# Performance work log

Hardware: AMD Instinct MI355X
Metric: run time of the kernel (lower is better)

## Reference

```python
import jax, jax.numpy as jnp
import numpy as np

DIM = 1024
HEAD_DIM = 64
CHUNK = 128
B, T = 4, 4096


def setup_inputs() -> dict:
    key = jax.random.key(0)
    ks = jax.random.split(key, 8)
    s = 1.0 / np.sqrt(DIM)
    inp = {
        'x': jax.random.normal(ks[0], (B, T, DIM), jnp.float32),
        'Wq': jax.random.normal(ks[1], (DIM, DIM), jnp.float32) * s,
        'bq': jnp.zeros((DIM,), jnp.float32),
        'Wk': jax.random.normal(ks[2], (DIM, DIM), jnp.float32) * s,
        'bk': jnp.zeros((DIM,), jnp.float32),
        'Wv': jax.random.normal(ks[3], (DIM, DIM), jnp.float32) * s,
        'bv': jnp.zeros((DIM,), jnp.float32),
        'Wbeta': jax.random.normal(ks[4], (DIM, DIM), jnp.float32) * s,
        'bbeta': jnp.zeros((DIM,), jnp.float32),
        'Walpha': jax.random.normal(ks[5], (DIM, DIM), jnp.float32) * s,
        'balpha': jnp.full((DIM,), 2.0, jnp.float32),  # bias init 2.0 as in torch
    }
    return inp


def reference(x, Wq, bq, Wk, bk, Wv, bv, Wbeta, bbeta, Walpha, balpha):
    Bsz, Tlen, D = x.shape
    d = HEAD_DIM
    H = D // d
    C = CHUNK
    scale = d ** (-0.5)

    q = ((x @ Wq.T + bq) * scale).reshape(Bsz, Tlen, H, d)
    k = ((x @ Wk.T + bk) * scale).reshape(Bsz, Tlen, H, d)
    v = (x @ Wv.T + bv).reshape(Bsz, Tlen, H, d)
    alpha_logits = jnp.clip((x @ Walpha.T + balpha).reshape(Bsz, Tlen, H, d), -10.0, 10.0)
    log_alpha = jax.nn.log_sigmoid(alpha_logits)
    alpha_val = jax.nn.sigmoid(alpha_logits)
    beta = jax.nn.softplus(x @ Wbeta.T + bbeta).reshape(Bsz, Tlen, H, d)

    # pad T to a multiple of C (static)
    pad = (-Tlen) % C
    if pad:
        pw = ((0, 0), (0, pad), (0, 0), (0, 0))
        q, k, v = jnp.pad(q, pw), jnp.pad(k, pw), jnp.pad(v, pw)
        log_alpha, beta = jnp.pad(log_alpha, pw), jnp.pad(beta, pw)
    N = q.shape[1] // C
    cshape = (Bsz, N, C, H, d)
    q, k, v = q.reshape(cshape), k.reshape(cshape), v.reshape(cshape)
    log_alpha, beta = log_alpha.reshape(cshape), beta.reshape(cshape)

    ccum = jnp.cumsum(log_alpha, axis=2)          # (B,N,C,H,d)
    m = ccum.mean(axis=-1)                        # (B,N,C,H); mean is linear -> take before pairwise diff
    decay_logits_mean = m[:, :, :, None, :] - m[:, :, None, :, :]  # (B,N,C,C,H)
    tril = jnp.tril(jnp.ones((C, C), jnp.float32))[None, None, :, :, None]
    decay_logits_mean = jnp.where(tril == 0, -1e9, decay_logits_mean)
    decay = jnp.exp(decay_logits_mean)            # (B,N,C,C,H)

    attn = jnp.einsum('bnihd,bnjhd->bnhij', q, k)
    attn = attn * decay.transpose(0, 1, 4, 2, 3)
    y_intra = jnp.einsum('bnhij,bnjhd->bnihd', attn, v * beta)  # (B,N,C,H,d)

    # inter-chunk recurrence via scan over chunks
    asum = jnp.exp(log_alpha.sum(axis=2).mean(axis=-1))  # (B,N,H) total chunk decay
    curve = jnp.exp(m)                                   # (B,N,C,H) intra-chunk decay curve
    bmean = beta.mean(axis=-1)                           # (B,N,C,H)

    def to_scan(a):
        return jnp.moveaxis(a, 1, 0)
    xs = (to_scan(q), to_scan(y_intra), to_scan(curve), to_scan(asum),
          to_scan(k), to_scan(v), to_scan(bmean))

    state0 = jnp.zeros((Bsz, H, d, d), jnp.float32)

    def step(state, inputs):
        qi, yi, ci, ai, ki, vi, bmi = inputs
        mem = jnp.einsum('bchq,bhqk->bchk', qi, state)
        y = yi + mem * ci[..., None]
        state = state * ai[:, :, None, None]
        delta = jnp.einsum('bchk,bchv,bch->bhkv', ki, vi, bmi)
        return state + delta, y

    state, ys = jax.lax.scan(step, state0, xs)
    y = jnp.moveaxis(ys, 0, 1).reshape(Bsz, N * C, D)
    if pad:
        y = y[:, :Tlen, :]
    return y, state, alpha_val
```

## Files before the change

kernel.cpp:

```cpp
#include <hip/hip_runtime.h>
#include <cstdint>
#include <cmath>

#define DIMM 1024
#define NHEAD 16
#define HEADD 64
#define CHUNKC 128
#define NBATCH 4
#define TLEN 4096
#define NCHUNK 32
#define BT (NBATCH * TLEN)
#define NSTACK (5 * DIMM)

typedef unsigned short ushort_t;
typedef __attribute__((ext_vector_type(8))) short short8;
typedef __attribute__((ext_vector_type(4))) float f32x4;

__device__ __forceinline__ float blo(unsigned int u) { return __uint_as_float(u << 16); }
__device__ __forceinline__ float bhi(unsigned int u) { return __uint_as_float(u & 0xffff0000u); }
__device__ __forceinline__ ushort_t f2bf(float f) {
  unsigned int u = __float_as_uint(f);
  u += 0x7fffu + ((u >> 16) & 1u);
  return (ushort_t)(u >> 16);
}
__device__ __forceinline__ float bf2f(ushort_t s) { return __uint_as_float(((unsigned int)s) << 16); }
__device__ __forceinline__ unsigned pack2(float a, float b) {
  return (unsigned)f2bf(a) | ((unsigned)f2bf(b) << 16);
}

__device__ __forceinline__ void stage16(unsigned lds_base, const ushort_t* g) {
  asm volatile("s_mov_b32 m0, %0\n\t"
               "global_load_lds_dwordx4 %1, off"
               :: "s"(lds_base), "v"((unsigned long long)(size_t)g)
               : "memory");
}

__global__ __launch_bounds__(256) void k_cast(
    const float* __restrict__ x,
    const float* __restrict__ Wq, const float* __restrict__ Wk,
    const float* __restrict__ Wv, const float* __restrict__ Wb, const float* __restrict__ Wa,
    const float* __restrict__ bq, const float* __restrict__ bk,
    const float* __restrict__ bv, const float* __restrict__ bb, const float* __restrict__ ba,
    ushort_t* __restrict__ xb, ushort_t* __restrict__ wbm, float* __restrict__ bias_st) {
  const long XU = (long)BT * DIMM / 4;
  const long WU = (long)NSTACK * DIMM / 4;
  const long BU = NSTACK / 4;
  const long NU = XU + WU + BU;
  for (long u = (long)blockIdx.x * blockDim.x + threadIdx.x; u < NU;
       u += (long)gridDim.x * blockDim.x) {
    if (u < XU) {
      float4 f = ((const float4*)x)[u];
      ushort4 o;
      o.x = f2bf(f.x); o.y = f2bf(f.y); o.z = f2bf(f.z); o.w = f2bf(f.w);
      ((ushort4*)xb)[u] = o;
    } else if (u < XU + WU) {
      long j = u - XU;
      long e = j * 4;
      int row = (int)(e >> 10);
      int col = (int)(e & 1023);
      int p = row >> 10, wr = row & 1023;
      const float* Wp = (p == 0) ? Wq : (p == 1) ? Wk : (p == 2) ? Wv : (p == 3) ? Wb : Wa;
      float4 f = *(const float4*)(Wp + (size_t)wr * DIMM + col);
      ushort4 o;
      o.x = f2bf(f.x); o.y = f2bf(f.y); o.z = f2bf(f.z); o.w = f2bf(f.w);
      ((ushort4*)wbm)[j] = o;
    } else {
      long j = u - XU - WU;
      int e = (int)(j * 4);
      int p = e >> 10, r = e & 1023;
      const float* bp = (p == 0) ? bq : (p == 1) ? bk : (p == 2) ? bv : (p == 3) ? bb : ba;
      ((float4*)bias_st)[j] = *(const float4*)(bp + r);
    }
  }
}

#define BARR __builtin_amdgcn_s_barrier()
#define VMC0 asm volatile("s_waitcnt vmcnt(0)" ::: "memory")

#define STAGEP(bb, kt) do {                                                      \
    const size_t _ko = (size_t)(kt) * 32;                                        \
    unsigned _base = (unsigned)__builtin_amdgcn_readfirstlane(                   \
        (int)(unsigned)(size_t)((__attribute__((address_space(3))) char*)smem    \
                                + (bb) * 16384 + wv1024));                       \
    stage16(_base,         agb + _ko);                                           \
    stage16(_base + 4096,  agb + (size_t)64 * DIMM + _ko);                       \
    stage16(_base + 8192,  bgb + _ko);                                           \
    stage16(_base + 12288, bgb + (size_t)64 * DIMM + _ko);                       \
  } while (0)

__global__ __launch_bounds__(256) void k_proj(
    const ushort_t* __restrict__ xb, const ushort_t* __restrict__ wbm,
    const float* __restrict__ bias_st,
    ushort_t* __restrict__ qo, ushort_t* __restrict__ ko,
    ushort_t* __restrict__ vo, ushort_t* __restrict__ bo,
    float* __restrict__ ao) {
  __shared__ __align__(16) char smem[32768];
  const int tid = threadIdx.x;
  const int lane = tid & 63;
  const int wave = tid >> 6;
  const int quad = lane >> 4, lr = lane & 15;
  const int wr = (wave >> 1) * 64, wc = (wave & 1) * 64;
  const int sx = (lr >> 1) & 3;
  const int wv1024 = wave * 1024;

  const int bm0 = blockIdx.y * 128, bn0 = blockIdx.x * 128;

  const int trow = tid >> 2;
  const int gcol = (((tid & 3) ^ ((tid >> 3) & 3)) << 3);
  const ushort_t* agb = xb + (size_t)(bm0 + trow) * DIMM + gcol;
  const ushort_t* bgb = wbm + (size_t)(bn0 + trow) * DIMM + gcol;

  f32x4 zero = {0.f, 0.f, 0.f, 0.f};
  f32x4 acc[4][4];
#pragma unroll
  for (int i = 0; i < 4; ++i)
#pragma unroll
    for (int j = 0; j < 4; ++j) acc[i][j] = zero;

  STAGEP(0, 0);

#pragma unroll 2
  for (int kk = 0; kk < 32; ++kk) {
    VMC0;
    BARR;
    if (kk < 31) STAGEP((kk + 1) & 1, kk + 1);
    const char* Ab = smem + (kk & 1) * 16384;
    const char* Bb = Ab + 8192;
    short8 af[4], bfr[4];
#pragma unroll
    for (int i = 0; i < 4; ++i)
      af[i] = *(const short8*)(Ab + (wr + i * 16 + lr) * 64 + ((quad ^ sx) << 4));
#pragma unroll
    for (int j = 0; j < 4; ++j)
      bfr[j] = *(const short8*)(Bb + (wc + j * 16 + lr) * 64 + ((quad ^ sx) << 4));
#pragma unroll
    for (int i = 0; i < 4; ++i)
#pragma unroll
      for (int j = 0; j < 4; ++j)
        acc[i][j] = __builtin_amdgcn_mfma_f32_16x16x32_bf16(af[i], bfr[j], acc[i][j], 0, 0, 0);
  }

  const int p_id = bn0 >> 10;
  const int ncol0 = bn0 & 1023;

  if (p_id == 4) {
#pragma unroll
    for (int j = 0; j < 4; ++j) {
      const int colg = wc + j * 16 + lr;
      const float bias = bias_st[bn0 + colg];
      const int nc = ncol0 + colg;
#pragma unroll
      for (int i = 0; i < 4; ++i)
#pragma unroll
        for (int r = 0; r < 4; ++r) {
          const int rowl = wr + i * 16 + quad * 4 + r;
          float val = acc[i][j][r] + bias;
          float c = fminf(fmaxf(val, -10.f), 10.f);
          ao[(size_t)(bm0 + rowl) * DIMM + nc] = 1.f / (1.f + expf(-c));
        }
    }
  } else {
    ushort_t* outp = (p_id == 0) ? qo : (p_id == 1) ? ko : (p_id == 2) ? vo : bo;
    const float scl = (p_id <= 1) ? 0.125f : 1.f;
    ushort_t* T = (ushort_t*)smem;
    const int halfb = (wr == 64) ? 32 : 0;
#pragma unroll
    for (int pass = 0; pass < 2; ++pass) {
      __syncthreads();
#pragma unroll
      for (int ii = 0; ii < 2; ++ii) {
        const int i = pass * 2 + ii;
#pragma unroll
        for (int j = 0; j < 4; ++j) {
          const int col = wc + j * 16 + lr;
          const float bias = bias_st[bn0 + col];
#pragma unroll
          for (int r = 0; r < 4; ++r) {
            float val = acc[i][j][r] + bias;
            float ov;
            if (p_id == 3) ov = (val > 20.f) ? val : log1pf(expf(val));
            else ov = val * scl;
            T[(halfb + ii * 16 + quad * 4 + r) * 136 + col] = f2bf(ov);
          }
        }
      }
      __syncthreads();
      const int trw = tid >> 2;
      const int cch = (tid & 3) * 32;
      const int growl = pass * 32 + (trw & 31) + (trw >> 5) * 64;
      ushort_t* dst = outp + (size_t)(bm0 + growl) * DIMM + ncol0 + cch;
      const ushort_t* src = T + trw * 136 + cch;
#pragma unroll
      for (int u = 0; u < 4; ++u)
        *(uint4*)(dst + u * 8) = *(const uint4*)(src + u * 8);
    }
  }
}

#undef STAGEP
#undef BARR
#undef VMC0

__global__ __launch_bounds__(128) void k_stats(
    const float* __restrict__ alpha, const ushort_t* __restrict__ betaw,
    float* __restrict__ mArr, float* __restrict__ bmean, float* __restrict__ asum) {
  const int bnh = blockIdx.x;
  const int h = bnh & 15, n = (bnh >> 4) & 31, b = bnh >> 9;
  const int c = threadIdx.x;
  const size_t bt = (size_t)b * TLEN + n * CHUNKC + c;

  const float4* ap = (const float4*)(alpha + bt * DIMM + h * HEADD);
  float ls = 0.f;
#pragma unroll
  for (int w = 0; w < 16; ++w) {
    float4 a = ap[w];
    ls += logf(a.x) + logf(a.y) + logf(a.z) + logf(a.w);
  }
  const uint4* bp = (const uint4*)(betaw + bt * DIMM + h * HEADD);
  float bs = 0.f;
#pragma unroll
  for (int w = 0; w < 8; ++w) {
    uint4 u = bp[w];
    bs += blo(u.x) + bhi(u.x) + blo(u.y) + bhi(u.y) + blo(u.z) + bhi(u.z) + blo(u.w) + bhi(u.w);
  }
  float la = ls * (1.f / 64.f);

  __shared__ float s[128];
  s[c] = la;
  __syncthreads();
  for (int off = 1; off < 128; off <<= 1) {
    float t = (c >= off) ? s[c - off] : 0.f;
    __syncthreads();
    s[c] += t;
    __syncthreads();
  }
  float m = s[c];
  const size_t o = (size_t)bnh * CHUNKC + c;
  mArr[o] = m;
  bmean[o] = bs * (1.f / 64.f);
  if (c == 127) asum[bnh] = expf(m);
}

__global__ __launch_bounds__(256) void k_delta(
    const ushort_t* __restrict__ kw, const ushort_t* __restrict__ vw,
    const float* __restrict__ bmean, float* __restrict__ delta) {
  __shared__ ushort_t kc[8192];
  __shared__ ushort_t vc[8192];
  __shared__ float bm[128];
  const int bnh = blockIdx.x;
  const int h = bnh & 15, n = (bnh >> 4) & 31, b = bnh >> 9;
  const int tid = threadIdx.x;
  const size_t bt0 = (size_t)b * TLEN + n * CHUNKC;

#pragma unroll
  for (int it = 0; it < 4; ++it) {
    int u = tid + it * 256;
    int row = u >> 3, col = (u & 7) * 8;
    size_t go = (bt0 + row) * DIMM + h * HEADD + col;
    ((uint4*)kc)[u] = *(const uint4*)(kw + go);
    ((uint4*)vc)[u] = *(const uint4*)(vw + go);
  }
  if (tid < 128) bm[tid] = bmean[(size_t)bnh * CHUNKC + tid];
  __syncthreads();

  const int kd = tid >> 2, v0 = (tid & 3) * 16;
  float acc[16];
#pragma unroll
  for (int l = 0; l < 16; ++l) acc[l] = 0.f;

#pragma unroll 4
  for (int c = 0; c < 128; ++c) {
    float kb = bf2f(kc[c * 64 + kd]) * bm[c];
    const uint4* vr = (const uint4*)(vc + c * 64 + v0);
    uint4 u0 = vr[0], u1 = vr[1];
    acc[0] += kb * blo(u0.x);  acc[1] += kb * bhi(u0.x);
    acc[2] += kb * blo(u0.y);  acc[3] += kb * bhi(u0.y);
    acc[4] += kb * blo(u0.z);  acc[5] += kb * bhi(u0.z);
    acc[6] += kb * blo(u0.w);  acc[7] += kb * bhi(u0.w);
    acc[8] += kb * blo(u1.x);  acc[9] += kb * bhi(u1.x);
    acc[10] += kb * blo(u1.y); acc[11] += kb * bhi(u1.y);
    acc[12] += kb * blo(u1.z); acc[13] += kb * bhi(u1.z);
    acc[14] += kb * blo(u1.w); acc[15] += kb * bhi(u1.w);
  }
  float* dst = delta + (size_t)bnh * 4096 + kd * 64 + v0;
#pragma unroll
  for (int l4 = 0; l4 < 4; ++l4)
    ((float4*)dst)[l4] = make_float4(acc[l4 * 4], acc[l4 * 4 + 1], acc[l4 * 4 + 2], acc[l4 * 4 + 3]);
}

__global__ __launch_bounds__(256) void k_scan(
    const float* __restrict__ delta, const float* __restrict__ asum,
    float* __restrict__ Earr, float* __restrict__ state_out) {
  const int bh = blockIdx.x >> 4;
  const int g = blockIdx.x & 15;
  const int b = bh >> 4, h = bh & 15;
  const int elem = g * 256 + threadIdx.x;
  float e = 0.f;
  for (int n = 0; n < 32; ++n) {
    const size_t o = (((size_t)b * 32 + n) * 16 + h) * 4096 + elem;
    const float a = asum[((size_t)b * 32 + n) * 16 + h];
    Earr[o] = e;
    e = e * a + delta[o];
  }
  state_out[(size_t)bh * 4096 + elem] = e;
}

__global__ __launch_bounds__(256) void k_y(
    const ushort_t* __restrict__ qw, const ushort_t* __restrict__ kw,
    const ushort_t* __restrict__ vw, const ushort_t* __restrict__ betaw,
    const float* __restrict__ mArr, const float* __restrict__ Earr,
    float* __restrict__ yout) {
  __shared__ __align__(16) ushort_t vbt[64][200];
  __shared__ __align__(16) ushort_t pst[4][32][40];
  __shared__ float ms[128];
  const int bnh = blockIdx.x;
  const int h = bnh & 15, n = (bnh >> 4) & 31, b = bnh >> 9;
  const int tid = threadIdx.x;
  const int lane = tid & 63;
  const int wv = tid >> 6;
  const int quad = lane >> 4, lr = lane & 15;
  const int i0 = wv * 32;
  const size_t bt0 = (size_t)b * TLEN + n * CHUNKC;
  const size_t hoff = (size_t)h * HEADD;

#pragma unroll
  for (int it = 0; it < 4; ++it) {
    int u = tid + it * 256;
    int j = u & 127, vd0 = (u >> 7) * 8;
    size_t go = (bt0 + j) * DIMM + hoff + vd0;
    uint4 vv = *(const uint4*)(vw + go);
    uint4 bb2 = *(const uint4*)(betaw + go);
    vbt[vd0 + 0][j] = f2bf(blo(vv.x) * blo(bb2.x));
    vbt[vd0 + 1][j] = f2bf(bhi(vv.x) * bhi(bb2.x));
    vbt[vd0 + 2][j] = f2bf(blo(vv.y) * blo(bb2.y));
    vbt[vd0 + 3][j] = f2bf(bhi(vv.y) * bhi(bb2.y));
    vbt[vd0 + 4][j] = f2bf(blo(vv.z) * blo(bb2.z));
    vbt[vd0 + 5][j] = f2bf(bhi(vv.z) * bhi(bb2.z));
    vbt[vd0 + 6][j] = f2bf(blo(vv.w) * blo(bb2.w));
    vbt[vd0 + 7][j] = f2bf(bhi(vv.w) * bhi(bb2.w));
  }
  const float4* Eg = (const float4*)(Earr + (size_t)bnh * 4096);
#pragma unroll
  for (int it = 0; it < 4; ++it) {
    int u = tid + it * 256;
    int kd = u >> 4, vd0 = (u & 15) * 4;
    float4 ev = Eg[u];
    vbt[vd0 + 0][128 + kd] = f2bf(ev.x);
    vbt[vd0 + 1][128 + kd] = f2bf(ev.y);
    vbt[vd0 + 2][128 + kd] = f2bf(ev.z);
    vbt[vd0 + 3][128 + kd] = f2bf(ev.w);
  }
  if (tid < 128) ms[tid] = mArr[(size_t)bnh * CHUNKC + tid];
  __syncthreads();

  short8 qa[2][2];
#pragma unroll
  for (int it = 0; it < 2; ++it) {
    const ushort_t* qg = qw + (bt0 + i0 + it * 16 + lr) * DIMM + hoff + quad * 8;
    qa[it][0] = *(const short8*)(qg);
    qa[it][1] = *(const short8*)(qg + 32);
  }
  float mi[2][4];
#pragma unroll
  for (int it = 0; it < 2; ++it)
#pragma unroll
    for (int r = 0; r < 4; ++r) mi[it][r] = ms[i0 + it * 16 + quad * 4 + r];

  f32x4 zero = {0.f, 0.f, 0.f, 0.f};
  f32x4 acc2[2][4];
#pragma unroll
  for (int it = 0; it < 2; ++it)
#pragma unroll
    for (int nt = 0; nt < 4; ++nt) acc2[it][nt] = zero;

  for (int js = 0; js < 4; ++js) {
    const int j0 = js * 32;
#pragma unroll
    for (int jsub = 0; jsub < 2; ++jsub) {
      const int j0s = j0 + jsub * 16;
      const ushort_t* kg = kw + (bt0 + j0s + lr) * DIMM + hoff + quad * 8;
      short8 kb0 = *(const short8*)(kg);
      short8 kb1 = *(const short8*)(kg + 32);
      const float mj = ms[j0s + lr];
#pragma unroll
      for (int it = 0; it < 2; ++it) {
        f32x4 s = __builtin_amdgcn_mfma_f32_16x16x32_bf16(qa[it][0], kb0, zero, 0, 0, 0);
        s = __builtin_amdgcn_mfma_f32_16x16x32_bf16(qa[it][1], kb1, s, 0, 0, 0);
#pragma unroll
        for (int r = 0; r < 4; ++r) {
          const int ig = i0 + it * 16 + quad * 4 + r;
          const int jg = j0s + lr;
          float w = (jg > ig) ? 0.f : s[r] * __expf(mi[it][r] - mj);
          pst[wv][it * 16 + quad * 4 + r][jsub * 16 + lr] = f2bf(w);
        }
      }
    }
#pragma unroll
    for (int it = 0; it < 2; ++it) {
      short8 pa = *(const short8*)&pst[wv][it * 16 + lr][quad * 8];
#pragma unroll
      for (int nt = 0; nt < 4; ++nt) {
        short8 vb = *(const short8*)&vbt[nt * 16 + lr][j0 + quad * 8];
        acc2[it][nt] = __builtin_amdgcn_mfma_f32_16x16x32_bf16(pa, vb, acc2[it][nt], 0, 0, 0);
      }
    }
  }

#pragma unroll
  for (int es = 0; es < 2; ++es) {
    const int kd0 = es * 32;
    {
      const int row = lane >> 1;
      const int col0 = (lane & 1) * 16;
      const float ex = __expf(ms[i0 + row]);
      const ushort_t* qg = qw + (bt0 + i0 + row) * DIMM + hoff + kd0 + col0;
      uint4 u0 = *(const uint4*)(qg);
      uint4 u1 = *(const uint4*)(qg + 8);
      uint4 w0, w1;
      w0.x = pack2(blo(u0.x) * ex, bhi(u0.x) * ex);
      w0.y = pack2(blo(u0.y) * ex, bhi(u0.y) * ex);
      w0.z = pack2(blo(u0.z) * ex, bhi(u0.z) * ex);
      w0.w = pack2(blo(u0.w) * ex, bhi(u0.w) * ex);
      w1.x = pack2(blo(u1.x) * ex, bhi(u1.x) * ex);
      w1.y = pack2(blo(u1.y) * ex, bhi(u1.y) * ex);
      w1.z = pack2(blo(u1.z) * ex, bhi(u1.z) * ex);
      w1.w = pack2(blo(u1.w) * ex, bhi(u1.w) * ex);
      *(uint4*)&pst[wv][row][col0] = w0;
      *(uint4*)&pst[wv][row][col0 + 8] = w1;
    }
#pragma unroll
    for (int it = 0; it < 2; ++it) {
      short8 pa = *(const short8*)&pst[wv][it * 16 + lr][quad * 8];
#pragma unroll
      for (int nt = 0; nt < 4; ++nt) {
        short8 vb = *(const short8*)&vbt[nt * 16 + lr][128 + kd0 + quad * 8];
        acc2[it][nt] = __builtin_amdgcn_mfma_f32_16x16x32_bf16(pa, vb, acc2[it][nt], 0, 0, 0);
      }
    }
  }

#pragma unroll
  for (int it = 0; it < 2; ++it) {
#pragma unroll
    for (int nt = 0; nt < 4; ++nt) {
      f32x4 a = acc2[it][nt];
#pragma unroll
      for (int r = 0; r < 4; ++r) {
        const int ig = i0 + it * 16 + quad * 4 + r;
        yout[(bt0 + ig) * DIMM + hoff + nt * 16 + lr] = a[r];
      }
    }
  }
}

extern "C" void kernel_launch(void* const* d_in, const int* in_sizes, int n_in,
                              void* d_out, int out_size, void* d_ws, size_t ws_size,
                              hipStream_t stream) {
  const float* x  = (const float*)d_in[0];
  const float* Wq = (const float*)d_in[1];
  const float* bq = (const float*)d_in[2];
  const float* Wk = (const float*)d_in[3];
  const float* bk = (const float*)d_in[4];
  const float* Wv = (const float*)d_in[5];
  const float* bv = (const float*)d_in[6];
  const float* Wb = (const float*)d_in[7];
  const float* bb = (const float*)d_in[8];
  const float* Wa = (const float*)d_in[9];
  const float* ba = (const float*)d_in[10];

  char* ws = (char*)d_ws;
  ushort_t* xb   = (ushort_t*)(ws + 0);
  ushort_t* wbm  = (ushort_t*)(ws + 33554432);
  float* bias_st = (float*)(ws + 44040192);
  ushort_t* qw   = (ushort_t*)(ws + 44060672);
  ushort_t* kw   = (ushort_t*)(ws + 77615104);
  ushort_t* vw   = (ushort_t*)(ws + 111169536);
  ushort_t* bw   = (ushort_t*)(ws + 144723968);
  float* mArr    = (float*)(ws + 178278400);
  float* bmean   = (float*)(ws + 179326976);
  float* asum    = (float*)(ws + 180375552);
  float* delta   = (float*)(ws + 180383744);
  float* Earr    = (float*)(ws + 213938176);

  float* yout = (float*)d_out;
  float* state_out = yout + (size_t)BT * DIMM;
  float* aout = state_out + (size_t)NBATCH * NHEAD * 64 * 64;

  k_cast<<<dim3(4096), dim3(256), 0, stream>>>(x, Wq, Wk, Wv, Wb, Wa,
                                               bq, bk, bv, bb, ba, xb, wbm, bias_st);
  k_proj<<<dim3(40, 128), dim3(256), 0, stream>>>(xb, wbm, bias_st, qw, kw, vw, bw, aout);
  k_stats<<<dim3(2048), dim3(128), 0, stream>>>(aout, bw, mArr, bmean, asum);
  k_delta<<<dim3(2048), dim3(256), 0, stream>>>(kw, vw, bmean, delta);
  k_scan<<<dim3(1024), dim3(256), 0, stream>>>(delta, asum, Earr, state_out);
  k_y<<<dim3(2048), dim3(256), 0, stream>>>(qw, kw, vw, bw, mArr, Earr, yout);
}
```

Measured before the change: 618.8 us.

## Compute chunk delta with bf16 MFMA and split projection launch in two

k_delta now pre-scales k by bmean, rounds it to bf16, and stores k and v transposed in a swizzled shared layout. It then computes the 64x64 k^T v outer-product sum with 16x16x32 bf16 MFMA instructions instead of scalar FMAs. The projection GEMM is also split into two launches over halves of the rows via a new ybase offset. Rounding k*bmean to bf16 adds a small precision loss, and the extra launch adds fixed overhead.

New measurement: 636.0 us. +2.8%, slower.

```diff
diff --git a/kernel.cpp b/kernel.cpp
--- a/kernel.cpp
+++ b/kernel.cpp
@@ -93,7 +93,7 @@
     const float* __restrict__ bias_st,
     ushort_t* __restrict__ qo, ushort_t* __restrict__ ko,
     ushort_t* __restrict__ vo, ushort_t* __restrict__ bo,
-    float* __restrict__ ao) {
+    float* __restrict__ ao, const int ybase) {
   __shared__ __align__(16) char smem[32768];
   const int tid = threadIdx.x;
   const int lane = tid & 63;
@@ -103,7 +103,7 @@
   const int sx = (lr >> 1) & 3;
   const int wv1024 = wave * 1024;
 
-  const int bm0 = blockIdx.y * 128, bn0 = blockIdx.x * 128;
+  const int bm0 = (blockIdx.y + ybase) * 128, bn0 = blockIdx.x * 128;
 
   const int trow = tid >> 2;
   const int gcol = (((tid & 3) ^ ((tid >> 3) & 3)) << 3);
@@ -244,48 +244,68 @@
 __global__ __launch_bounds__(256) void k_delta(
     const ushort_t* __restrict__ kw, const ushort_t* __restrict__ vw,
     const float* __restrict__ bmean, float* __restrict__ delta) {
-  __shared__ ushort_t kc[8192];
-  __shared__ ushort_t vc[8192];
-  __shared__ float bm[128];
+  __shared__ __align__(16) ushort_t kt[4][64][32];
+  __shared__ __align__(16) ushort_t vt[4][64][32];
   const int bnh = blockIdx.x;
   const int h = bnh & 15, n = (bnh >> 4) & 31, b = bnh >> 9;
   const int tid = threadIdx.x;
+  const int lane = tid & 63;
+  const int wv = tid >> 6;
+  const int quad = lane >> 4, lr = lane & 15;
+  const int sx = (lr >> 1) & 3;
   const size_t bt0 = (size_t)b * TLEN + n * CHUNKC;
 
 #pragma unroll
   for (int it = 0; it < 4; ++it) {
-    int u = tid + it * 256;
-    int row = u >> 3, col = (u & 7) * 8;
-    size_t go = (bt0 + row) * DIMM + h * HEADD + col;
-    ((uint4*)kc)[u] = *(const uint4*)(kw + go);
-    ((uint4*)vc)[u] = *(const uint4*)(vw + go);
-  }
-  if (tid < 128) bm[tid] = bmean[(size_t)bnh * CHUNKC + tid];
+    const int u = tid + it * 256;
+    const int c = u >> 3;
+    const int d0 = (u & 7) * 8;
+    const size_t go = (bt0 + c) * DIMM + h * HEADD + d0;
+    uint4 k4 = *(const uint4*)(kw + go);
+    uint4 v4 = *(const uint4*)(vw + go);
+    const float bmc = bmean[(size_t)bnh * CHUNKC + c];
+    const int ks = c >> 5, cc = c & 31;
+    const int csl = cc >> 3, ce = cc & 7;
+    ushort_t kv[8], vv8[8];
+    kv[0] = f2bf(blo(k4.x) * bmc); kv[1] = f2bf(bhi(k4.x) * bmc);
+    kv[2] = f2bf(blo(k4.y) * bmc); kv[3] = f2bf(bhi(k4.y) * bmc);
+    kv[4] = f2bf(blo(k4.z) * bmc); kv[5] = f2bf(bhi(k4.z) * bmc);
+    kv[6] = f2bf(blo(k4.w) * bmc); kv[7] = f2bf(bhi(k4.w) * bmc);
+    vv8[0] = (ushort_t)(v4.x & 0xffffu); vv8[1] = (ushort_t)(v4.x >> 16);
+    vv8[2] = (ushort_t)(v4.y & 0xffffu); vv8[3] = (ushort_t)(v4.y >> 16);
+    vv8[4] = (ushort_t)(v4.z & 0xffffu); vv8[5] = (ushort_t)(v4.z >> 16);
+    vv8[6] = (ushort_t)(v4.w & 0xffffu); vv8[7] = (ushort_t)(v4.w >> 16);
+#pragma unroll
+    for (int j = 0; j < 8; ++j) {
+      const int d = d0 + j;
+      const int ph = (csl ^ ((d >> 1) & 3)) * 8 + ce;
+      kt[ks][d][ph] = kv[j];
+      vt[ks][d][ph] = vv8[j];
+    }
+  }
   __syncthreads();
 
-  const int kd = tid >> 2, v0 = (tid & 3) * 16;
-  float acc[16];
-#pragma unroll
-  for (int l = 0; l < 16; ++l) acc[l] = 0.f;
-
-#pragma unroll 4
-  for (int c = 0; c < 128; ++c) {
-    float kb = bf2f(kc[c * 64 + kd]) * bm[c];
-    const uint4* vr = (const uint4*)(vc + c * 64 + v0);
-    uint4 u0 = vr[0], u1 = vr[1];
-    acc[0] += kb * blo(u0.x);  acc[1] += kb * bhi(u0.x);
-    acc[2] += kb * blo(u0.y);  acc[3] += kb * bhi(u0.y);
-    acc[4] += kb * blo(u0.z);  acc[5] += kb * bhi(u0.z);
-    acc[6] += kb * blo(u0.w);  acc[7] += kb * bhi(u0.w);
-    acc[8] += kb * blo(u1.x);  acc[9] += kb * bhi(u1.x);
-    acc[10] += kb * blo(u1.y); acc[11] += kb * bhi(u1.y);
-    acc[12] += kb * blo(u1.z); acc[13] += kb * bhi(u1.z);
-    acc[14] += kb * blo(u1.w); acc[15] += kb * bhi(u1.w);
-  }
-  float* dst = delta + (size_t)bnh * 4096 + kd * 64 + v0;
-#pragma unroll
-  for (int l4 = 0; l4 < 4; ++l4)
-    ((float4*)dst)[l4] = make_float4(acc[l4 * 4], acc[l4 * 4 + 1], acc[l4 * 4 + 2], acc[l4 * 4 + 3]);
+  f32x4 zero = {0.f, 0.f, 0.f, 0.f};
+  f32x4 acc[4];
+#pragma unroll
+  for (int nt = 0; nt < 4; ++nt) acc[nt] = zero;
+
+#pragma unroll
+  for (int ks = 0; ks < 4; ++ks) {
+    short8 af = *(const short8*)&kt[ks][wv * 16 + lr][(quad ^ sx) * 8];
+#pragma unroll
+    for (int nt = 0; nt < 4; ++nt) {
+      short8 bf = *(const short8*)&vt[ks][nt * 16 + lr][(quad ^ sx) * 8];
+      acc[nt] = __builtin_amdgcn_mfma_f32_16x16x32_bf16(af, bf, acc[nt], 0, 0, 0);
+    }
+  }
+
+  float* dst = delta + (size_t)bnh * 4096;
+#pragma unroll
+  for (int nt = 0; nt < 4; ++nt)
+#pragma unroll
+    for (int r = 0; r < 4; ++r)
+      dst[(wv * 16 + quad * 4 + r) * 64 + nt * 16 + lr] = acc[nt][r];
 }
 
 __global__ __launch_bounds__(256) void k_scan(
@@ -488,7 +508,8 @@
 
   k_cast<<<dim3(4096), dim3(256), 0, stream>>>(x, Wq, Wk, Wv, Wb, Wa,
                                                bq, bk, bv, bb, ba, xb, wbm, bias_st);
-  k_proj<<<dim3(40, 128), dim3(256), 0, stream>>>(xb, wbm, bias_st, qw, kw, vw, bw, aout);
+  k_proj<<<dim3(40, 64), dim3(256), 0, stream>>>(xb, wbm, bias_st, qw, kw, vw, bw, aout, 0);
+  k_proj<<<dim3(40, 64), dim3(256), 0, stream>>>(xb, wbm, bias_st, qw, kw, vw, bw, aout, 64);
   k_stats<<<dim3(2048), dim3(128), 0, stream>>>(aout, bw, mArr, bmean, asum);
   k_delta<<<dim3(2048), dim3(256), 0, stream>>>(kw, vw, bmean, delta);
   k_scan<<<dim3(1024), dim3(256), 0, stream>>>(delta, asum, Earr, state_out);
```
